# Kernel tuning notes

Hardware: AMD Instinct MI355X
Metric: run time of the kernel (lower is better)

## Reference

```python
import jax, jax.numpy as jnp
import numpy as np

P = 16; D = 1024; NH = 16; MAG = 4
B = 2; V = 4; H = 256; W = 512
DEPTH = 6; NE = 2; NM = 3   # dense-early, sparse-middle, rest dense-late
L = (H // P) * (W // P)    # 512 tokens
KEEP = L // 4              # keep_ratio = 0.25 -> 128 hard tokens
HD = D // NH
SCALE = HD ** -0.5


def setup_inputs() -> dict:
    key = jax.random.key(0)
    ks = iter(jax.random.split(key, 64))
    def rn(shape, s=0.02):
        return jax.random.normal(next(ks), shape, jnp.float32) * s
    inp = {}
    inp['x'] = jax.random.normal(next(ks), (B, V, H, W), jnp.float32)
    # select_hard_tokens: per-row randperm(L)[:K], sorted -> deterministic input
    rng = np.random.default_rng(0)
    hi = np.stack([np.sort(rng.permutation(L)[:KEEP]) for _ in range(B)]).astype(np.int32)
    inp['hard_idx'] = jnp.asarray(hi)
    inp['patch_w'] = rn((V, P * P, D)); inp['patch_b'] = jnp.zeros((V, D), jnp.float32)
    inp['var_embed'] = rn((V, D)); inp['var_query'] = rn((D,))
    inp['agg_wq'] = rn((D, D)); inp['agg_wk'] = rn((D, D))
    inp['agg_wv'] = rn((D, D)); inp['agg_wo'] = rn((D, D))
    inp['agg_bo'] = jnp.zeros((D,), jnp.float32)
    inp['pos_embed'] = rn((L, D), 1.0)
    inp['ln1_w'] = jnp.ones((DEPTH, D), jnp.float32); inp['ln1_b'] = jnp.zeros((DEPTH, D), jnp.float32)
    inp['qkv_w'] = rn((DEPTH, D, 3 * D)); inp['qkv_b'] = jnp.zeros((DEPTH, 3 * D), jnp.float32)
    inp['aproj_w'] = rn((DEPTH, D, D)); inp['aproj_b'] = jnp.zeros((DEPTH, D), jnp.float32)
    inp['ln2_w'] = jnp.ones((DEPTH, D), jnp.float32); inp['ln2_b'] = jnp.zeros((DEPTH, D), jnp.float32)
    inp['fc1_w'] = rn((DEPTH, D, 4 * D)); inp['fc1_b'] = jnp.zeros((DEPTH, 4 * D), jnp.float32)
    inp['fc2_w'] = rn((DEPTH, 4 * D, D)); inp['fc2_b'] = jnp.zeros((DEPTH, D), jnp.float32)
    inp['norm_w'] = jnp.ones((D,), jnp.float32); inp['norm_b'] = jnp.zeros((D,), jnp.float32)
    inp['head_w'] = rn((2, D, D)); inp['head_b'] = jnp.zeros((2, D), jnp.float32)
    inp['head_out_w'] = rn((D, (MAG * P) ** 2)); inp['head_out_b'] = jnp.zeros(((MAG * P) ** 2,), jnp.float32)
    inp['p2c1_w'] = rn((4 * MAG * MAG, V, 3, 3)); inp['p2c1_b'] = jnp.zeros((4 * MAG * MAG,), jnp.float32)
    inp['p2c2_w'] = rn((1, 4, 3, 3)); inp['p2c2_b'] = jnp.zeros((1,), jnp.float32)
    inp['cout_w'] = rn((1, 1, 3, 3)); inp['cout_b'] = jnp.zeros((1,), jnp.float32)
    return inp


def _ln(x, g, b):
    m = jnp.mean(x, -1, keepdims=True)
    v = jnp.mean((x - m) ** 2, -1, keepdims=True)
    return (x - m) * jax.lax.rsqrt(v + 1e-5) * g + b


def _conv3x3(x, w, b):
    y = jax.lax.conv_general_dilated(x, w, (1, 1), 'SAME',
                                     dimension_numbers=('NCHW', 'OIHW', 'NCHW'))
    return y + b[None, :, None, None]


def _pixel_shuffle(x, r):
    b, c, h, w = x.shape
    c2 = c // (r * r)
    return x.reshape(b, c2, r, r, h, w).transpose(0, 1, 4, 2, 5, 3).reshape(b, c2, h * r, w * r)


def _block_step(c, p):
    l1w, l1b, qw, qb, pw, pb, l2w, l2b, f1w, f1b, f2w, f2b = p
    bsz, n, _ = c.shape
    hn = _ln(c, l1w, l1b)
    qkv = (hn @ qw + qb).reshape(bsz, n, 3, NH, HD).transpose(2, 0, 3, 1, 4)  # 3,b,h,n,d
    qh, kh, vh = qkv[0], qkv[1], qkv[2]
    att = jax.nn.softmax(jnp.einsum('bhqd,bhkd->bhqk', qh, kh) * SCALE, axis=-1)
    o = jnp.einsum('bhqk,bhkd->bhqd', att, vh).transpose(0, 2, 1, 3).reshape(bsz, n, D)
    c = c + o @ pw + pb
    hn2 = _ln(c, l2w, l2b)
    c = c + jax.nn.gelu(hn2 @ f1w + f1b, approximate=False) @ f2w + f2b
    return c, None


def reference(x, hard_idx, patch_w, patch_b, var_embed, var_query,
              agg_wq, agg_wk, agg_wv, agg_wo, agg_bo, pos_embed,
              ln1_w, ln1_b, qkv_w, qkv_b, aproj_w, aproj_b,
              ln2_w, ln2_b, fc1_w, fc1_b, fc2_w, fc2_b,
              norm_w, norm_b, head_w, head_b, head_out_w, head_out_b,
              p2c1_w, p2c1_b, p2c2_w, p2c2_b, cout_w, cout_b):
    b_, v_, h_img, w_img = x.shape
    hh, ww = h_img // P, w_img // P
    ltok = hh * ww
    # per-variable patch embedding (PatchEmbed with in_chans=1)
    xp = x.reshape(b_, v_, hh, P, ww, P).transpose(0, 1, 2, 4, 3, 5).reshape(b_, v_, ltok, P * P)
    tok = jnp.einsum('bvle,ved->bvld', xp, patch_w) + patch_b[None, :, None, :]
    tok = tok + var_embed[None, :, None, :]
    # aggregate_variables: cross-attention query over V per token
    xf = tok.transpose(0, 2, 1, 3).reshape(b_ * ltok, v_, D)
    q = (var_query @ agg_wq).reshape(NH, HD)
    k = (xf @ agg_wk).reshape(-1, v_, NH, HD)
    vv = (xf @ agg_wv).reshape(-1, v_, NH, HD)
    a = jax.nn.softmax(jnp.einsum('hd,nvhd->nhv', q, k) * SCALE, axis=-1)
    agg = jnp.einsum('nhv,nvhd->nhd', a, vv).reshape(-1, D) @ agg_wo + agg_bo
    xt = agg.reshape(b_, ltok, D) + pos_embed[None]
    stacked = (ln1_w, ln1_b, qkv_w, qkv_b, aproj_w, aproj_b,
               ln2_w, ln2_b, fc1_w, fc1_b, fc2_w, fc2_b)
    def run(c, s, e):
        c, _ = jax.lax.scan(_block_step, c, tuple(ar[s:e] for ar in stacked))
        return c
    # dense early blocks (all tokens)
    xt = run(xt, 0, NE)
    # gather hard tokens -> sparse middle blocks; easy tokens skip via identity
    hard = jnp.take_along_axis(xt, hard_idx[:, :, None].astype(jnp.int32), axis=1)
    hard = run(hard, NE, NE + NM)
    brow = jnp.arange(b_)[:, None]
    xt = xt.at[brow, hard_idx].set(hard)  # merge_tokens (easy = identity)
    # dense late blocks
    xt = run(xt, NE + NM, DEPTH)
    xt = _ln(xt, norm_w, norm_b)
    # decoder head
    for i in range(head_w.shape[0]):
        xt = jax.nn.gelu(xt @ head_w[i] + head_b[i], approximate=False)
    pred = xt @ head_out_w + head_out_b  # (B, L, (MAG*P)^2)
    # unpatchify with scaling=MAG
    h2, w2 = h_img * MAG // P, w_img * MAG // P
    y = pred.reshape(b_, h2, w2, P, P, 1)
    y = jnp.einsum('nhwpqc->nchpwq', y).reshape(b_, 1, h2 * P, w2 * P)
    # residual path2 on raw input channels (out_var_index = all 4 channels here)
    r = jax.nn.gelu(_conv3x3(x, p2c1_w, p2c1_b), approximate=False)
    r = _pixel_shuffle(r, MAG)
    r = _conv3x3(r, p2c2_w, p2c2_b)
    return _conv3x3(y + r, cout_w, cout_b)
```

## Files before the change

### kernel.cpp

```cpp
#include <hip/hip_runtime.h>
#include <math.h>


#define UNIT 1048576L

typedef __attribute__((ext_vector_type(8))) short short8;
typedef __attribute__((ext_vector_type(4))) float f32x4;

#define GLDS(gp, lp) __builtin_amdgcn_global_load_lds( \
    (const __attribute__((address_space(1))) void*)(gp), \
    (__attribute__((address_space(3))) void*)(lp), 16, 0, 0)

__device__ __forceinline__ float gelu_f(float v){
  return 0.5f*v*(1.0f + erff(v*0.70710678118654752440f));
}

__device__ __forceinline__ unsigned short f2bf(float f){
  union { float f; unsigned u; } a; a.f = f;
  unsigned r = a.u + 0x7fffu + ((a.u >> 16) & 1u);
  return (unsigned short)(r >> 16);
}
__device__ __forceinline__ float bf2f(unsigned short u){
  union { unsigned u; float f; } a; a.u = (unsigned)u << 16;
  return a.f;
}

struct WJobs {
  const float* W[4];
  unsigned short* T[4];
  int K[4], N[4];
  int start[4];
};

__global__ __launch_bounds__(256)
void wtrans_multi(WJobs J)
{
  __shared__ float tile[32][33];
  int bx = blockIdx.x;
  int j = 0;
  #pragma unroll
  for (int i = 1; i < 4; ++i) if (bx >= J.start[i]) j = i;
  int local = bx - J.start[j];
  int K = J.K[j], N = J.N[j];
  int nx = N >> 5, tpb = (K >> 5) * nx;
  int bz = local / tpb, rem = local % tpb;
  int k0 = (rem / nx) * 32, n0 = (rem % nx) * 32;
  const float* Wp = J.W[j] + (long)bz * K * N;
  unsigned short* Wo = J.T[j] + (long)bz * K * N;
  int tx = threadIdx.x & 31, ty = threadIdx.x >> 5;
  #pragma unroll
  for (int i = 0; i < 4; ++i)
    tile[ty*4+i][tx] = Wp[(long)(k0 + ty*4 + i)*N + n0 + tx];
  __syncthreads();
  #pragma unroll
  for (int i = 0; i < 4; ++i){
    int n = ty*4 + i;
    Wo[(long)(n0 + n)*K + k0 + tx] = f2bf(tile[tx][n]);
  }
}

template<int TM>
__global__ __launch_bounds__(256)
void gemm_bt(const unsigned short* __restrict__ A, const unsigned short* __restrict__ Wt,
             const float* __restrict__ bias, const float* __restrict__ res,
             float* __restrict__ Cf, unsigned short* __restrict__ Cb,
             float* __restrict__ Cp, long MN, int splits,
             int M, int N, int K, int ldc,
             long sA, long sW, long sBias, long sRes, long sC,
             int wmod, int act)
{
  constexpr int NJ = (TM == 128) ? 4 : 2;
  int bz0 = blockIdx.z;
  int sp = bz0 % splits, bz = bz0 / splits;
  A += (long)bz * sA;
  int wb = bz % wmod;
  Wt += (long)wb * sW;
  const float* bptr = bias ? bias + (long)wb * sBias : nullptr;
  const float* rptr = res  ? res  + (long)bz * sRes : nullptr;
  if (Cf) Cf += (long)bz * sC;
  if (Cb) Cb += (long)bz * sC;

  __shared__ __align__(16) unsigned short As[TM*32];
  __shared__ __align__(16) unsigned short Bs[128*32];

  int t = threadIdx.x;
  int wave = t >> 6, lane = t & 63;
  int ln = lane & 15, kg = lane >> 4;
  int wm, wn;
  if (TM == 128){ wm = (wave & 1) * 64; wn = (wave >> 1) * 64; }
  else          { wm = 0;               wn = wave * 32; }
  int row0 = blockIdx.y * TM, col0 = blockIdx.x * 128;

  f32x4 acc[4][NJ];
  f32x4 z = {0.f, 0.f, 0.f, 0.f};
  #pragma unroll
  for (int i = 0; i < 4; ++i)
    #pragma unroll
    for (int j = 0; j < NJ; ++j) acc[i][j] = z;

  int sm = t >> 2;
  int sk = (t & 3) * 8;
  unsigned short* AsB = As + wave*512;
  unsigned short* BsB = Bs + wave*512;

  int kpb = K / splits;
  int kbeg = sp * kpb, kend = kbeg + kpb;
  for (int k0 = kbeg; k0 < kend; k0 += 32){
    if (TM == 128){
      GLDS(&A[(long)(row0 + sm)*K + k0 + sk],      AsB);
      GLDS(&A[(long)(row0 + 64 + sm)*K + k0 + sk], AsB + 2048);
    } else {
      GLDS(&A[(long)(row0 + sm)*K + k0 + sk],      AsB);
    }
    GLDS(&Wt[(long)(col0 + sm)*K + k0 + sk],      BsB);
    GLDS(&Wt[(long)(col0 + 64 + sm)*K + k0 + sk], BsB + 2048);
    __syncthreads();
    short8 af[4], bfg[NJ];
    #pragma unroll
    for (int i = 0; i < 4; ++i)  af[i]  = *(const short8*)&As[(wm + i*16 + ln)*32 + kg*8];
    #pragma unroll
    for (int j = 0; j < NJ; ++j) bfg[j] = *(const short8*)&Bs[(wn + j*16 + ln)*32 + kg*8];
    #pragma unroll
    for (int i = 0; i < 4; ++i)
      #pragma unroll
      for (int j = 0; j < NJ; ++j)
        acc[i][j] = __builtin_amdgcn_mfma_f32_16x16x32_bf16(af[i], bfg[j], acc[i][j], 0, 0, 0);
    __syncthreads();
  }

  if (Cp){
    long nbat = gridDim.z / splits;
    float* P = Cp + ((long)sp*nbat + bz)*MN;
    #pragma unroll
    for (int i = 0; i < 4; ++i){
      int rbase = row0 + wm + i*16 + kg*4;
      #pragma unroll
      for (int j = 0; j < NJ; ++j){
        int c = col0 + wn + j*16 + ln;
        #pragma unroll
        for (int rr2 = 0; rr2 < 4; ++rr2)
          P[(long)(rbase + rr2)*ldc + c] = acc[i][j][rr2];
      }
    }
    return;
  }
  #pragma unroll
  for (int i = 0; i < 4; ++i){
    int rbase = row0 + wm + i*16 + kg*4;
    #pragma unroll
    for (int j = 0; j < NJ; ++j){
      int c = col0 + wn + j*16 + ln;
      float bv = bptr ? bptr[c] : 0.f;
      #pragma unroll
      for (int rr2 = 0; rr2 < 4; ++rr2){
        int rrow = rbase + rr2;
        float v = acc[i][j][rr2] + bv;
        if (rptr) v += rptr[(long)rrow*ldc + c];
        if (act == 1) v = gelu_f(v);
        if (Cf) Cf[(long)rrow*ldc + c] = v;
        if (Cb) Cb[(long)rrow*ldc + c] = f2bf(v);
      }
    }
  }
}

__global__ __launch_bounds__(256)
void reduce_ep(const float* __restrict__ Cp, int splits, int nbat, long MN, int N,
               const float* __restrict__ bias, const float* __restrict__ res, long sRes,
               float* __restrict__ Cf, unsigned short* __restrict__ Cb, long sC, int act)
{
  long e4 = (long)blockIdx.x*256 + threadIdx.x;
  if (e4 >= (long)nbat*MN/4) return;
  long e = e4 * 4;
  int b = (int)(e / MN); long r = e % MN; int col = (int)(r % N);
  float4 s = *(const float4*)&Cp[(long)b*MN + r];
  for (int sp = 1; sp < splits; ++sp){
    float4 p = *(const float4*)&Cp[((long)sp*nbat + b)*MN + r];
    s.x += p.x; s.y += p.y; s.z += p.z; s.w += p.w;
  }
  if (bias){
    float4 bv = *(const float4*)&bias[col];
    s.x += bv.x; s.y += bv.y; s.z += bv.z; s.w += bv.w;
  }
  if (res){
    float4 rv = *(const float4*)&res[(long)b*sRes + r];
    s.x += rv.x; s.y += rv.y; s.z += rv.z; s.w += rv.w;
  }
  if (act == 1){
    s.x = gelu_f(s.x); s.y = gelu_f(s.y); s.z = gelu_f(s.z); s.w = gelu_f(s.w);
  }
  if (Cf) *(float4*)&Cf[(long)b*sC + r] = s;
  if (Cb){
    unsigned q0 = (unsigned)f2bf(s.x) | ((unsigned)f2bf(s.y) << 16);
    unsigned q1 = (unsigned)f2bf(s.z) | ((unsigned)f2bf(s.w) << 16);
    uint2 pk = {q0, q1};
    *(uint2*)&Cb[(long)b*sC + r] = pk;
  }
}

__global__ __launch_bounds__(256)
void ln_bf(const float* __restrict__ x, const float* __restrict__ g,
           const float* __restrict__ b, unsigned short* __restrict__ y)
{
  long r = blockIdx.x;
  int t = threadIdx.x;
  float4 v = ((const float4*)(x + r*1024))[t];
  float s  = v.x + v.y + v.z + v.w;
  float ss = v.x*v.x + v.y*v.y + v.z*v.z + v.w*v.w;
  #pragma unroll
  for (int o = 32; o; o >>= 1){ s += __shfl_xor(s, o); ss += __shfl_xor(ss, o); }
  __shared__ float sa[4], sb[4];
  int w = t >> 6, lane = t & 63;
  if (!lane){ sa[w] = s; sb[w] = ss; }
  __syncthreads();
  s  = sa[0] + sa[1] + sa[2] + sa[3];
  ss = sb[0] + sb[1] + sb[2] + sb[3];
  float mean = s * (1.0f/1024.0f);
  float var  = ss * (1.0f/1024.0f) - mean*mean;
  float rstd = rsqrtf(var + 1e-5f);
  float4 gv = ((const float4*)g)[t];
  float4 bv = ((const float4*)b)[t];
  float ox = (v.x-mean)*rstd*gv.x + bv.x;
  float oy = (v.y-mean)*rstd*gv.y + bv.y;
  float oz = (v.z-mean)*rstd*gv.z + bv.z;
  float ow = (v.w-mean)*rstd*gv.w + bv.w;
  unsigned q0 = (unsigned)f2bf(ox) | ((unsigned)f2bf(oy) << 16);
  unsigned q1 = (unsigned)f2bf(oz) | ((unsigned)f2bf(ow) << 16);
  uint2 pk = {q0, q1};
  *(uint2*)&y[r*1024 + t*4] = pk;
}

__global__ void xp_extract(const float* __restrict__ x, unsigned short* __restrict__ xp)
{
  int idx = blockIdx.x * 256 + threadIdx.x;
  int e4 = idx & 63;
  int lt = (idx >> 6) & 511;
  int zz = idx >> 15;
  int e  = e4 << 2;
  int py = e >> 4, px0 = e & 15;
  int hy = lt >> 5, wx = lt & 31;
  float4 v = *(const float4*)&x[((long)zz*256 + hy*16 + py)*512 + wx*16 + px0];
  unsigned q0 = (unsigned)f2bf(v.x) | ((unsigned)f2bf(v.y) << 16);
  unsigned q1 = (unsigned)f2bf(v.z) | ((unsigned)f2bf(v.w) << 16);
  uint2 pk = {q0, q1};
  ((uint2*)xp)[idx] = pk;
}

__global__ void pb2_combine(const float* __restrict__ pb, const float* __restrict__ ve,
                            float* __restrict__ out)
{
  int i = blockIdx.x * 256 + threadIdx.x;
  out[i] = pb[i] + ve[i];
}

__global__ void qproj(const float* __restrict__ vq, const float* __restrict__ wq,
                      float* __restrict__ q)
{
  int n = blockIdx.x * 64 + threadIdx.x;
  float s = 0.f;
  for (int k = 0; k < 1024; ++k) s += vq[k] * wq[(long)k*1024 + n];
  q[n] = s;
}

__global__ void wk_fold(const float* __restrict__ wk, const float* __restrict__ qv,
                        float* __restrict__ wt)
{
  int i = blockIdx.x * 256 + threadIdx.x;
  int h = i & 15, D = i >> 4;
  const float* wr = wk + (long)D*1024 + h*64;
  const float* qr = qv + h*64;
  float s = 0.f;
  #pragma unroll
  for (int d = 0; d < 64; ++d) s += wr[d]*qr[d];
  wt[h*1024 + D] = s;
}

__global__ __launch_bounds__(64)
void agg_attn2(const unsigned short* __restrict__ tok, const float* __restrict__ vb,
               const float* __restrict__ wt, unsigned short* __restrict__ out)
{
  int l = blockIdx.x, h = blockIdx.y, b = blockIdx.z, t = threadIdx.x;
  const float* wh = wt + h*1024;
  float sc[4];
  #pragma unroll
  for (int v = 0; v < 4; ++v){
    const unsigned short* tr = tok + ((((long)b*4 + v)*512 + l) << 10);
    float s = 0.f;
    #pragma unroll
    for (int j = 0; j < 16; ++j){
      int D = t + j*64;
      s += bf2f(tr[D]) * wh[D];
    }
    #pragma unroll
    for (int o = 32; o; o >>= 1) s += __shfl_xor(s, o);
    sc[v] = s * 0.125f;
  }
  float m = fmaxf(fmaxf(sc[0], sc[1]), fmaxf(sc[2], sc[3]));
  float e0 = __expf(sc[0]-m), e1 = __expf(sc[1]-m), e2 = __expf(sc[2]-m), e3 = __expf(sc[3]-m);
  float inv = 1.0f / (e0 + e1 + e2 + e3);
  long base = (((long)b*4)*512 + l)*1024 + h*64 + t;
  float o = e0*vb[base] + e1*vb[base + 512*1024] + e2*vb[base + 2*512*1024] + e3*vb[base + 3*512*1024];
  out[(((long)b*512 + l) << 10) + h*64 + t] = f2bf(o * inv);
}

__global__ __launch_bounds__(256)
void attn_v2(const float* __restrict__ qkv, unsigned short* __restrict__ out, int N)
{
  int h = blockIdx.y, b = blockIdx.z;
  int row0 = blockIdx.x * 32;
  int t = threadIdx.x;
  int r = t & 31, g = t >> 5;
  int c0 = g * 8;
  const float* base = qkv + (long)b * N * 3072;

  __shared__ float QsT[64][33];
  __shared__ float KV[64][68];
  __shared__ float Ps[32][65];
  __shared__ float red[32][9], red2[32][9];

  {
    const float* qp = base + (long)(row0 + r)*3072 + h*64 + c0;
    float4 a  = *(const float4*)qp;
    float4 bq = *(const float4*)(qp + 4);
    QsT[c0+0][r]=a.x;  QsT[c0+1][r]=a.y;  QsT[c0+2][r]=a.z;  QsT[c0+3][r]=a.w;
    QsT[c0+4][r]=bq.x; QsT[c0+5][r]=bq.y; QsT[c0+6][r]=bq.z; QsT[c0+7][r]=bq.w;
  }
  float m_r = -1e30f, l_r = 0.f;
  float O[8] = {0,0,0,0,0,0,0,0};
  int vc = t & 63, vd = (t >> 6) * 16;

  for (int j0 = 0; j0 < N; j0 += 64){
    __syncthreads();
    {
      const float* kp = base + (long)(j0 + vc)*3072 + 1024 + h*64 + vd;
      float4 k1 = *(const float4*)kp,     k2 = *(const float4*)(kp+4);
      float4 k3 = *(const float4*)(kp+8), k4 = *(const float4*)(kp+12);
      KV[vd+ 0][vc]=k1.x; KV[vd+ 1][vc]=k1.y; KV[vd+ 2][vc]=k1.z; KV[vd+ 3][vc]=k1.w;
      KV[vd+ 4][vc]=k2.x; KV[vd+ 5][vc]=k2.y; KV[vd+ 6][vc]=k2.z; KV[vd+ 7][vc]=k2.w;
      KV[vd+ 8][vc]=k3.x; KV[vd+ 9][vc]=k3.y; KV[vd+10][vc]=k3.z; KV[vd+11][vc]=k3.w;
      KV[vd+12][vc]=k4.x; KV[vd+13][vc]=k4.y; KV[vd+14][vc]=k4.z; KV[vd+15][vc]=k4.w;
    }
    __syncthreads();
    float s[8] = {0,0,0,0,0,0,0,0};
    #pragma unroll 16
    for (int d = 0; d < 64; ++d){
      float q = QsT[d][r];
      float4 k1 = *(const float4*)&KV[d][c0];
      float4 k2 = *(const float4*)&KV[d][c0+4];
      s[0] += q*k1.x; s[1] += q*k1.y; s[2] += q*k1.z; s[3] += q*k1.w;
      s[4] += q*k2.x; s[5] += q*k2.y; s[6] += q*k2.z; s[7] += q*k2.w;
    }
    float lm = -1e30f;
    #pragma unroll
    for (int i = 0; i < 8; ++i){ s[i] *= 0.125f; lm = fmaxf(lm, s[i]); }
    red[r][g] = lm;
    __syncthreads();
    float mc = red[r][0];
    #pragma unroll
    for (int gg = 1; gg < 8; ++gg) mc = fmaxf(mc, red[r][gg]);
    float m_new = fmaxf(m_r, mc);
    float alpha = __expf(m_r - m_new);
    float ls = 0.f;
    #pragma unroll
    for (int i = 0; i < 8; ++i){ float p = __expf(s[i]-m_new); Ps[r][c0+i] = p; ls += p; }
    red2[r][g] = ls;
    __syncthreads();
    float cs = 0.f;
    #pragma unroll
    for (int gg = 0; gg < 8; ++gg) cs += red2[r][gg];
    l_r = alpha*l_r + cs;
    m_r = m_new;
    #pragma unroll
    for (int i = 0; i < 8; ++i) O[i] *= alpha;
    {
      const float* vp = base + (long)(j0 + vc)*3072 + 2048 + h*64 + vd;
      float4 v1 = *(const float4*)vp,     v2 = *(const float4*)(vp+4);
      float4 v3 = *(const float4*)(vp+8), v4 = *(const float4*)(vp+12);
      *(float4*)&KV[vc][vd]    = v1;
      *(float4*)&KV[vc][vd+4]  = v2;
      *(float4*)&KV[vc][vd+8]  = v3;
      *(float4*)&KV[vc][vd+12] = v4;
    }
    __syncthreads();
    #pragma unroll 16
    for (int j = 0; j < 64; ++j){
      float p = Ps[r][j];
      float4 v1 = *(const float4*)&KV[j][c0];
      float4 v2 = *(const float4*)&KV[j][c0+4];
      O[0] += p*v1.x; O[1] += p*v1.y; O[2] += p*v1.z; O[3] += p*v1.w;
      O[4] += p*v2.x; O[5] += p*v2.y; O[6] += p*v2.z; O[7] += p*v2.w;
    }
  }
  float inv = 1.0f / l_r;
  unsigned q0 = (unsigned)f2bf(O[0]*inv) | ((unsigned)f2bf(O[1]*inv) << 16);
  unsigned q1 = (unsigned)f2bf(O[2]*inv) | ((unsigned)f2bf(O[3]*inv) << 16);
  unsigned q2 = (unsigned)f2bf(O[4]*inv) | ((unsigned)f2bf(O[5]*inv) << 16);
  unsigned q3 = (unsigned)f2bf(O[6]*inv) | ((unsigned)f2bf(O[7]*inv) << 16);
  uint4 pk = {q0, q1, q2, q3};
  *(uint4*)&out[((long)(b*N + row0 + r))*1024 + h*64 + c0] = pk;
}

__global__ __launch_bounds__(256)
void gather_rows(const float* __restrict__ src, const int* __restrict__ idx,
                 float* __restrict__ dst)
{
  int r = blockIdx.x;
  int b = r >> 7, i = r & 127;
  int s = idx[b*128 + i];
  ((float4*)(dst + (long)r*1024))[threadIdx.x] =
      ((const float4*)(src + ((long)b*512 + s)*1024))[threadIdx.x];
}
__global__ __launch_bounds__(256)
void scatter_rows(const float* __restrict__ src, const int* __restrict__ idx,
                  float* __restrict__ dst)
{
  int r = blockIdx.x;
  int b = r >> 7, i = r & 127;
  int s = idx[b*128 + i];
  ((float4*)(dst + ((long)b*512 + s)*1024))[threadIdx.x] =
      ((const float4*)(src + (long)r*1024))[threadIdx.x];
}

__global__ __launch_bounds__(256)
void conv1_v4(const float* __restrict__ x, const float* __restrict__ w,
              const float* __restrict__ bi, unsigned short* __restrict__ out)
{
  __shared__ unsigned short obuf[256*68];
  int t = threadIdx.x;
  int id = blockIdx.x*256 + t;
  int px = id & 511, py = (id >> 9) & 255, bb = id >> 17;
  float in[4][9];
  #pragma unroll
  for (int ci = 0; ci < 4; ++ci){
    const float* xc = x + ((long)(bb*4 + ci)*256)*512;
    #pragma unroll
    for (int ky = 0; ky < 3; ++ky){
      int yy = py + ky - 1;
      #pragma unroll
      for (int kx = 0; kx < 3; ++kx){
        int xx = px + kx - 1;
        bool ok = ((unsigned)yy < 256u) && ((unsigned)xx < 512u);
        in[ci][ky*3+kx] = ok ? xc[yy*512 + xx] : 0.f;
      }
    }
  }
  unsigned short* orow = &obuf[t*68];
  #pragma unroll 2
  for (int g = 0; g < 8; ++g){
    unsigned pk[4];
    #pragma unroll
    for (int u = 0; u < 8; ++u){
      int co = g*8 + u;
      float s = bi[co];
      #pragma unroll
      for (int ci = 0; ci < 4; ++ci){
        const float* wc = w + (co*4 + ci)*9;
        #pragma unroll
        for (int k = 0; k < 9; ++k) s += in[ci][k]*wc[k];
      }
      s = gelu_f(s);
      unsigned short h = f2bf(s);
      if (u & 1) pk[u>>1] |= ((unsigned)h << 16);
      else       pk[u>>1]  = (unsigned)h;
    }
    uint2 v0 = {pk[0], pk[1]};
    uint2 v1 = {pk[2], pk[3]};
    *(uint2*)&orow[g*8]     = v0;
    *(uint2*)&orow[g*8 + 4] = v1;
  }
  __syncthreads();
  unsigned short* ob = out + (long)blockIdx.x * (256*64);
  #pragma unroll
  for (int j = 0; j < 8; ++j){
    int u = j*256 + t;
    int p = u >> 3, s4 = u & 7;
    uint2 a  = *(const uint2*)&obuf[p*68 + s4*8];
    uint2 b2 = *(const uint2*)&obuf[p*68 + s4*8 + 4];
    uint4 v = {a.x, a.y, b2.x, b2.y};
    *(uint4*)&ob[(long)u*8] = v;
  }
}

__global__ __launch_bounds__(256)
void conv2_v3(const unsigned short* __restrict__ r1, const float* __restrict__ w,
              const float* __restrict__ bi, float* __restrict__ out)
{
  __shared__ float cbuf[108*68];
  int X0 = blockIdx.x*64, Y0 = blockIdx.y*16, bb = blockIdx.z;
  int cx0 = (X0 >> 2) - 1, cy0 = (Y0 >> 2) - 1;
  int t = threadIdx.x;
  const unsigned short* rb = r1 + (long)bb*256*512*64;
  for (int i4 = t; i4 < 1728; i4 += 256){
    int cell = i4 >> 4, ch4 = (i4 & 15) << 2;
    int cy = cy0 + cell/18, cx = cx0 + cell%18;
    float4 v = {0.f, 0.f, 0.f, 0.f};
    if ((unsigned)cy < 256u && (unsigned)cx < 512u){
      uint2 u = *(const uint2*)&rb[(((long)cy*512 + cx) << 6) + ch4];
      v.x = bf2f((unsigned short)(u.x & 0xffff));
      v.y = bf2f((unsigned short)(u.x >> 16));
      v.z = bf2f((unsigned short)(u.y & 0xffff));
      v.w = bf2f((unsigned short)(u.y >> 16));
    }
    *(float4*)&cbuf[cell*68 + ch4] = v;
  }
  float wv[36];
  #pragma unroll
  for (int k = 0; k < 36; ++k) wv[k] = w[k];
  float bias = bi[0];
  __syncthreads();
  int lx = t & 63, tq = t >> 6;
  int X = X0 + lx;
  #pragma unroll
  for (int j = 0; j < 4; ++j){
    int Y = Y0 + tq*4 + j;
    float s = bias;
    #pragma unroll
    for (int ky = 0; ky < 3; ++ky){
      int yy = Y + ky - 1;
      if ((unsigned)yy >= 1024u) continue;
      int ly = (yy >> 2) - cy0, phy = (yy & 3) << 2;
      #pragma unroll
      for (int kx = 0; kx < 3; ++kx){
        int xx = X + kx - 1;
        if ((unsigned)xx >= 2048u) continue;
        int lxc = (xx >> 2) - cx0;
        const float* cp = &cbuf[(ly*18 + lxc)*68 + phy + (xx & 3)];
        s += cp[0]*wv[ky*3+kx] + cp[16]*wv[9+ky*3+kx]
           + cp[32]*wv[18+ky*3+kx] + cp[48]*wv[27+ky*3+kx];
      }
    }
    out[(((long)bb*1024 + Y) << 11) + X] = s;
  }
}

__global__ __launch_bounds__(256)
void cout_fused(const float* __restrict__ pred, const float* __restrict__ r2,
                const float* __restrict__ w, const float* __restrict__ bi,
                float* __restrict__ out)
{
  __shared__ float tb[18*66];
  int X0 = blockIdx.x*64, Y0 = blockIdx.y*16, bb = blockIdx.z;
  int t = threadIdx.x;
  for (int i = t; i < 1188; i += 256){
    int ly = i/66, lx = i%66;
    int Y = Y0 + ly - 1, X = X0 + lx - 1;
    float v = 0.f;
    if ((unsigned)Y < 1024u && (unsigned)X < 2048u){
      int i2 = Y >> 4, p = Y & 15, j2 = X >> 4, q = X & 15;
      int l = i2*8 + (j2 >> 4);
      int e = ((j2 & 15) << 8) + (p << 4) + q;
      v = pred[(((long)bb*512 + l) << 12) + e] + r2[(((long)bb*1024 + Y) << 11) + X];
    }
    tb[i] = v;
  }
  float w0=w[0], w1=w[1], w2=w[2], w3=w[3], w4=w[4], w5=w[5], w6=w[6], w7=w[7], w8=w[8];
  float bias = bi[0];
  __syncthreads();
  int lx = t & 63, tq = t >> 6;
  #pragma unroll
  for (int j = 0; j < 4; ++j){
    int ry = tq*4 + j;
    const float* c = &tb[ry*66 + lx];
    float s = bias + c[0]*w0 + c[1]*w1 + c[2]*w2
            + c[66]*w3 + c[67]*w4 + c[68]*w5
            + c[132]*w6 + c[133]*w7 + c[134]*w8;
    out[(((long)bb*1024 + Y0 + ry) << 11) + X0 + lx] = s;
  }
}

static inline void gemm_go(hipStream_t st, int TM, const unsigned short* A,
                           const unsigned short* Wt,
                           const float* bias, const float* res, float* Cf, unsigned short* Cb,
                           float* Cp, int splits,
                           int M, int N, int K, int batches,
                           long sA, long sW, long sBias, long sRes, long sC,
                           int wmod, int act)
{
  dim3 g(N/128, M/TM, batches*splits);
  long MN = (long)M*N;
  if (TM == 128)
    gemm_bt<128><<<g, 256, 0, st>>>(A, Wt, bias, res, Cf, Cb, Cp, MN, splits,
                                    M, N, K, N, sA, sW, sBias, sRes, sC, wmod, act);
  else
    gemm_bt<64><<<g, 256, 0, st>>>(A, Wt, bias, res, Cf, Cb, Cp, MN, splits,
                                   M, N, K, N, sA, sW, sBias, sRes, sC, wmod, act);
}

static inline void reduce_go(hipStream_t st, const float* Cp, int splits, int nbat,
                             long MN, int N, const float* bias, const float* res, long sRes,
                             float* Cf, unsigned short* Cb, long sC, int act)
{
  long total4 = (long)nbat*MN/4;
  reduce_ep<<<(int)((total4 + 255)/256), 256, 0, st>>>(Cp, splits, nbat, MN, N,
                                                       bias, res, sRes, Cf, Cb, sC, act);
}

static inline void wmulti_go(hipStream_t st, int njobs,
                             const float* W0, unsigned short* T0, int K0, int N0, int nb0,
                             const float* W1, unsigned short* T1, int K1, int N1, int nb1,
                             const float* W2, unsigned short* T2, int K2, int N2, int nb2,
                             const float* W3, unsigned short* T3, int K3, int N3, int nb3)
{
  WJobs J;
  const float* Ws[4] = {W0, W1, W2, W3};
  unsigned short* Ts[4] = {T0, T1, T2, T3};
  int Ks[4] = {K0, K1, K2, K3}, Ns[4] = {N0, N1, N2, N3}, nbs[4] = {nb0, nb1, nb2, nb3};
  int acc = 0;
  for (int i = 0; i < 4; ++i){
    if (i < njobs){
      J.W[i] = Ws[i]; J.T[i] = Ts[i]; J.K[i] = Ks[i]; J.N[i] = Ns[i];
      J.start[i] = acc;
      acc += nbs[i] * (Ks[i] >> 5) * (Ns[i] >> 5);
    } else {
      J.W[i] = Ws[0]; J.T[i] = Ts[0]; J.K[i] = 32; J.N[i] = 32;
      J.start[i] = 0x7fffffff;
    }
  }
  wtrans_multi<<<acc, 256, 0, st>>>(J);
}

extern "C" void kernel_launch(void* const* d_in, const int* in_sizes, int n_in,
                              void* d_out, int out_size, void* d_ws, size_t ws_size,
                              hipStream_t stream)
{
  const float* x         = (const float*)d_in[0];
  const int*   hard_idx  = (const int*)  d_in[1];
  const float* patch_w   = (const float*)d_in[2];
  const float* patch_b   = (const float*)d_in[3];
  const float* var_embed = (const float*)d_in[4];
  const float* var_query = (const float*)d_in[5];
  const float* agg_wq    = (const float*)d_in[6];
  const float* agg_wk    = (const float*)d_in[7];
  const float* agg_wv    = (const float*)d_in[8];
  const float* agg_wo    = (const float*)d_in[9];
  const float* agg_bo    = (const float*)d_in[10];
  const float* pos_embed = (const float*)d_in[11];
  const float* ln1_w     = (const float*)d_in[12];
  const float* ln1_b     = (const float*)d_in[13];
  const float* qkv_w     = (const float*)d_in[14];
  const float* qkv_b     = (const float*)d_in[15];
  const float* aproj_w   = (const float*)d_in[16];
  const float* aproj_b   = (const float*)d_in[17];
  const float* ln2_w     = (const float*)d_in[18];
  const float* ln2_b     = (const float*)d_in[19];
  const float* fc1_w     = (const float*)d_in[20];
  const float* fc1_b     = (const float*)d_in[21];
  const float* fc2_w     = (const float*)d_in[22];
  const float* fc2_b     = (const float*)d_in[23];
  const float* norm_w    = (const float*)d_in[24];
  const float* norm_b    = (const float*)d_in[25];
  const float* head_w    = (const float*)d_in[26];
  const float* head_b    = (const float*)d_in[27];
  const float* head_out_w= (const float*)d_in[28];
  const float* head_out_b= (const float*)d_in[29];
  const float* p2c1_w    = (const float*)d_in[30];
  const float* p2c1_b    = (const float*)d_in[31];
  const float* p2c2_w    = (const float*)d_in[32];
  const float* p2c2_b    = (const float*)d_in[33];
  const float* cout_w    = (const float*)d_in[34];
  const float* cout_b    = (const float*)d_in[35];

  float* ws = (float*)d_ws;
  float* xt   = ws;
  float* r2   = ws + 1*UNIT;
  float* qkvb = ws + 5*UNIT;
  float* pred = ws + 8*UNIT;
  unsigned short* rbig = (unsigned short*)(ws + 8*UNIT);
  float* vb   = ws + 12*UNIT;
  float* Cp   = ws + 12*UNIT;
  unsigned short* b16 = (unsigned short*)(ws + 16*UNIT);
  unsigned short* hn_bf    = b16;
  unsigned short* ao_bf    = b16 + 1*UNIT;
  unsigned short* ff_bf    = b16 + 2*UNIT;
  unsigned short* xp_bf    = b16 + 6*UNIT;
  unsigned short* tok_bf   = b16 + 7*UNIT;
  unsigned short* aggin_bf = b16 + 11*UNIT;
  unsigned short* wt_a     = b16 + 12*UNIT;
  float* tail = ws + 28*UNIT;
  float* pb2  = tail;
  float* qv   = tail + 4096;
  float* wtl  = tail + 5120;
  float* hbuf = tail + 21504;

  conv1_v4<<<1024, 256, 0, stream>>>(x, p2c1_w, p2c1_b, rbig);
  conv2_v3<<<dim3(32, 64, 2), 256, 0, stream>>>(rbig, p2c2_w, p2c2_b, r2);

  unsigned short* wt_patch = wt_a;
  unsigned short* wt_wv    = wt_a + 1*UNIT;
  unsigned short* wt_wo    = wt_a + 2*UNIT;
  pb2_combine<<<16, 256, 0, stream>>>(patch_b, var_embed, pb2);
  xp_extract<<<1024, 256, 0, stream>>>(x, xp_bf);
  qproj<<<16, 64, 0, stream>>>(var_query, agg_wq, qv);
  wk_fold<<<64, 256, 0, stream>>>(agg_wk, qv, wtl);
  wmulti_go(stream, 3,
            patch_w, wt_patch, 256, 1024, 4,
            agg_wv,  wt_wv,   1024, 1024, 1,
            agg_wo,  wt_wo,   1024, 1024, 1,
            nullptr, nullptr, 0, 0, 0);
  gemm_go(stream, 128, xp_bf, wt_patch, pb2, nullptr, nullptr, tok_bf, nullptr, 1,
          512, 1024, 256, 8, 512L*256, 256L*1024, 1024, 0, 512L*1024, 4, 0);
  gemm_go(stream, 128, tok_bf, wt_wv, nullptr, nullptr, vb, nullptr, nullptr, 1,
          512, 1024, 1024, 8, 512L*1024, 0, 0, 0, 512L*1024, 1, 0);
  agg_attn2<<<dim3(512, 16, 2), 64, 0, stream>>>(tok_bf, vb, wtl, aggin_bf);
  gemm_go(stream, 64, aggin_bf, wt_wo, nullptr, nullptr, nullptr, nullptr, Cp, 2,
          512, 1024, 1024, 2, 512L*1024, 0, 0, 0, 512L*1024, 1, 0);
  reduce_go(stream, Cp, 2, 2, 512L*1024, 1024, agg_bo, pos_embed, 0, xt, nullptr,
            512L*1024, 0);

  unsigned short* wt_qkv   = wt_a;
  unsigned short* wt_aproj = wt_a + 3*UNIT;
  unsigned short* wt_fc1   = wt_a + 4*UNIT;
  unsigned short* wt_fc2   = wt_a + 8*UNIT;

  auto run_block = [&](float* cur, int Nt, int d){
    int rows = 2 * Nt;
    bool dense = (rows >= 1024);
    int TMbig = dense ? 128 : 64;
    long MNq = (long)rows*3072, MNa = (long)rows*1024, MNf = (long)rows*4096;
    wmulti_go(stream, 4,
              qkv_w   + (long)d*1024*3072, wt_qkv,   1024, 3072, 1,
              aproj_w + (long)d*1024*1024, wt_aproj, 1024, 1024, 1,
              fc1_w   + (long)d*1024*4096, wt_fc1,   1024, 4096, 1,
              fc2_w   + (long)d*4096*1024, wt_fc2,   4096, 1024, 1);
    ln_bf<<<rows, 256, 0, stream>>>(cur, ln1_w + d*1024, ln1_b + d*1024, hn_bf);
    gemm_go(stream, TMbig, hn_bf, wt_qkv, qkv_b + d*3072, nullptr, qkvb, nullptr, nullptr, 1,
            rows, 3072, 1024, 1, 0, 0, 0, 0, 0, 1, 0);
    attn_v2<<<dim3(Nt/32, 16, 2), 256, 0, stream>>>(qkvb, ao_bf, Nt);
    {
      int sk = dense ? 4 : 8;
      gemm_go(stream, TMbig, ao_bf, wt_aproj, nullptr, nullptr, nullptr, nullptr, Cp, sk,
              rows, 1024, 1024, 1, 0, 0, 0, 0, 0, 1, 0);
      reduce_go(stream, Cp, sk, 1, MNa, 1024, aproj_b + d*1024, cur, MNa, cur, nullptr, MNa, 0);
    }
    ln_bf<<<rows, 256, 0, stream>>>(cur, ln2_w + d*1024, ln2_b + d*1024, hn_bf);
    if (dense){
      gemm_go(stream, 128, hn_bf, wt_fc1, fc1_b + d*4096, nullptr, nullptr, ff_bf, nullptr, 1,
              rows, 4096, 1024, 1, 0, 0, 0, 0, 0, 1, 1);
    } else {
      gemm_go(stream, 64, hn_bf, wt_fc1, nullptr, nullptr, nullptr, nullptr, Cp, 2,
              rows, 4096, 1024, 1, 0, 0, 0, 0, 0, 1, 1);
      reduce_go(stream, Cp, 2, 1, MNf, 4096, fc1_b + d*4096, nullptr, 0, nullptr, ff_bf, MNf, 1);
    }
    {
      int sk = dense ? 4 : 8;
      gemm_go(stream, TMbig, ff_bf, wt_fc2, nullptr, nullptr, nullptr, nullptr, Cp, sk,
              rows, 1024, 4096, 1, 0, 0, 0, 0, 0, 1, 0);
      reduce_go(stream, Cp, sk, 1, MNa, 1024, fc2_b + d*1024, cur, MNa, cur, nullptr, MNa, 0);
    }
  };

  run_block(xt, 512, 0);
  run_block(xt, 512, 1);
  gather_rows<<<256, 256, 0, stream>>>(xt, hard_idx, hbuf);
  run_block(hbuf, 128, 2);
  run_block(hbuf, 128, 3);
  run_block(hbuf, 128, 4);
  scatter_rows<<<256, 256, 0, stream>>>(hbuf, hard_idx, xt);
  run_block(xt, 512, 5);

  unsigned short* wt_h1 = wt_a;
  unsigned short* wt_h2 = wt_a + 1*UNIT;
  unsigned short* wt_ho = wt_a + 2*UNIT;
  wmulti_go(stream, 3,
            head_w,              wt_h1, 1024, 1024, 1,
            head_w + 1024L*1024, wt_h2, 1024, 1024, 1,
            head_out_w,          wt_ho, 1024, 4096, 1,
            nullptr, nullptr, 0, 0, 0);
  ln_bf<<<1024, 256, 0, stream>>>(xt, norm_w, norm_b, hn_bf);
  gemm_go(stream, 64, hn_bf, wt_h1, nullptr, nullptr, nullptr, nullptr, Cp, 2,
          1024, 1024, 1024, 1, 0, 0, 0, 0, 0, 1, 1);
  reduce_go(stream, Cp, 2, 1, 1024L*1024, 1024, head_b, nullptr, 0, nullptr, ao_bf,
            1024L*1024, 1);
  gemm_go(stream, 64, ao_bf, wt_h2, nullptr, nullptr, nullptr, nullptr, Cp, 2,
          1024, 1024, 1024, 1, 0, 0, 0, 0, 0, 1, 1);
  reduce_go(stream, Cp, 2, 1, 1024L*1024, 1024, head_b + 1024, nullptr, 0, nullptr, hn_bf,
            1024L*1024, 1);
  gemm_go(stream, 128, hn_bf, wt_ho, head_out_b, nullptr, pred, nullptr, nullptr, 1,
          1024, 4096, 1024, 1, 0, 0, 0, 0, 0, 1, 0);

  cout_fused<<<dim3(32, 64, 2), 256, 0, stream>>>(pred, r2, cout_w, cout_b, (float*)d_out);
}
```

Baseline: 1.574 ms.

## Rewrite attention with bf16 MFMA and split-KV across waves

Replaces the scalar fp32 flash-attention kernel with one that converts Q, K and V to bf16 and computes QK^T and PV with 16x16x32 MFMA instructions. Each block processes 128-key tiles, and pairs of waves split the key range; their partial softmax states are merged through shared memory at the end. This removes the fp32 FMA inner loops and several block-wide reductions per tile. In exchange it adds bf16 rounding of the attention inputs and probabilities, plus a strided transpose store of V into LDS that may cause bank conflicts.

```diff
diff --git a/kernel.cpp b/kernel.cpp
--- a/kernel.cpp
+++ b/kernel.cpp
@@ -304,100 +304,155 @@
 }
 
 __global__ __launch_bounds__(256)
-void attn_v2(const float* __restrict__ qkv, unsigned short* __restrict__ out, int N)
+void attn_mfma(const float* __restrict__ qkv, unsigned short* __restrict__ out, int N)
 {
   int h = blockIdx.y, b = blockIdx.z;
   int row0 = blockIdx.x * 32;
   int t = threadIdx.x;
-  int r = t & 31, g = t >> 5;
-  int c0 = g * 8;
+  int wave = t >> 6, lane = t & 63;
+  int ln = lane & 15, kg = lane >> 4;
+  int mtile = wave & 1, khalf = wave >> 1;
   const float* base = qkv + (long)b * N * 3072;
 
-  __shared__ float QsT[64][33];
-  __shared__ float KV[64][68];
-  __shared__ float Ps[32][65];
-  __shared__ float red[32][9], red2[32][9];
-
+  __shared__ __align__(16) unsigned short Ks[128*72];
+  __shared__ __align__(16) unsigned short Vt[64*136];
+  __shared__ __align__(16) unsigned short Pw[4][16*72];
+  __shared__ float Obuf[4][16][68];
+  __shared__ float Mbuf[4][16], Lbuf[4][16];
+
+  short8 qf[2];
   {
-    const float* qp = base + (long)(row0 + r)*3072 + h*64 + c0;
-    float4 a  = *(const float4*)qp;
-    float4 bq = *(const float4*)(qp + 4);
-    QsT[c0+0][r]=a.x;  QsT[c0+1][r]=a.y;  QsT[c0+2][r]=a.z;  QsT[c0+3][r]=a.w;
-    QsT[c0+4][r]=bq.x; QsT[c0+5][r]=bq.y; QsT[c0+6][r]=bq.z; QsT[c0+7][r]=bq.w;
-  }
-  float m_r = -1e30f, l_r = 0.f;
-  float O[8] = {0,0,0,0,0,0,0,0};
-  int vc = t & 63, vd = (t >> 6) * 16;
-
-  for (int j0 = 0; j0 < N; j0 += 64){
+    const float* qp = base + (long)(row0 + mtile*16 + ln)*3072 + h*64;
+    #pragma unroll
+    for (int s = 0; s < 2; ++s){
+      float4 a = *(const float4*)(qp + s*32 + kg*8);
+      float4 c = *(const float4*)(qp + s*32 + kg*8 + 4);
+      short8 q;
+      q[0] = (short)f2bf(a.x*0.125f); q[1] = (short)f2bf(a.y*0.125f);
+      q[2] = (short)f2bf(a.z*0.125f); q[3] = (short)f2bf(a.w*0.125f);
+      q[4] = (short)f2bf(c.x*0.125f); q[5] = (short)f2bf(c.y*0.125f);
+      q[6] = (short)f2bf(c.z*0.125f); q[7] = (short)f2bf(c.w*0.125f);
+      qf[s] = q;
+    }
+  }
+
+  f32x4 z = {0.f, 0.f, 0.f, 0.f};
+  f32x4 O[4] = {z, z, z, z};
+  float mrow[4] = {-1e30f, -1e30f, -1e30f, -1e30f};
+  float lrow[4] = {0.f, 0.f, 0.f, 0.f};
+  unsigned short* pw = &Pw[wave][0];
+
+  for (int j0 = 0; j0 < N; j0 += 128){
+    #pragma unroll
+    for (int it = 0; it < 2; ++it){
+      int key = (t >> 2) + it*64;
+      int dg = (t & 3) * 16;
+      const float* kp = base + (long)(j0 + key)*3072 + 1024 + h*64 + dg;
+      float4 k0 = *(const float4*)kp,     k1 = *(const float4*)(kp+4);
+      float4 k2 = *(const float4*)(kp+8), k3 = *(const float4*)(kp+12);
+      unsigned short* kd = &Ks[key*72 + dg];
+      uint2 p0 = { (unsigned)f2bf(k0.x) | ((unsigned)f2bf(k0.y)<<16),
+                   (unsigned)f2bf(k0.z) | ((unsigned)f2bf(k0.w)<<16) };
+      uint2 p1 = { (unsigned)f2bf(k1.x) | ((unsigned)f2bf(k1.y)<<16),
+                   (unsigned)f2bf(k1.z) | ((unsigned)f2bf(k1.w)<<16) };
+      uint2 p2 = { (unsigned)f2bf(k2.x) | ((unsigned)f2bf(k2.y)<<16),
+                   (unsigned)f2bf(k2.z) | ((unsigned)f2bf(k2.w)<<16) };
+      uint2 p3 = { (unsigned)f2bf(k3.x) | ((unsigned)f2bf(k3.y)<<16),
+                   (unsigned)f2bf(k3.z) | ((unsigned)f2bf(k3.w)<<16) };
+      *(uint2*)&kd[0]  = p0; *(uint2*)&kd[4]  = p1;
+      *(uint2*)&kd[8]  = p2; *(uint2*)&kd[12] = p3;
+      const float* vp = base + (long)(j0 + key)*3072 + 2048 + h*64 + dg;
+      float4 v0 = *(const float4*)vp,     v1 = *(const float4*)(vp+4);
+      float4 v2 = *(const float4*)(vp+8), v3 = *(const float4*)(vp+12);
+      float vv[16];
+      vv[0]=v0.x; vv[1]=v0.y; vv[2]=v0.z; vv[3]=v0.w;
+      vv[4]=v1.x; vv[5]=v1.y; vv[6]=v1.z; vv[7]=v1.w;
+      vv[8]=v2.x; vv[9]=v2.y; vv[10]=v2.z; vv[11]=v2.w;
+      vv[12]=v3.x; vv[13]=v3.y; vv[14]=v3.z; vv[15]=v3.w;
+      #pragma unroll
+      for (int i = 0; i < 16; ++i) Vt[(dg+i)*136 + key] = f2bf(vv[i]);
+    }
     __syncthreads();
-    {
-      const float* kp = base + (long)(j0 + vc)*3072 + 1024 + h*64 + vd;
-      float4 k1 = *(const float4*)kp,     k2 = *(const float4*)(kp+4);
-      float4 k3 = *(const float4*)(kp+8), k4 = *(const float4*)(kp+12);
-      KV[vd+ 0][vc]=k1.x; KV[vd+ 1][vc]=k1.y; KV[vd+ 2][vc]=k1.z; KV[vd+ 3][vc]=k1.w;
-      KV[vd+ 4][vc]=k2.x; KV[vd+ 5][vc]=k2.y; KV[vd+ 6][vc]=k2.z; KV[vd+ 7][vc]=k2.w;
-      KV[vd+ 8][vc]=k3.x; KV[vd+ 9][vc]=k3.y; KV[vd+10][vc]=k3.z; KV[vd+11][vc]=k3.w;
-      KV[vd+12][vc]=k4.x; KV[vd+13][vc]=k4.y; KV[vd+14][vc]=k4.z; KV[vd+15][vc]=k4.w;
+
+    f32x4 acc[4] = {z, z, z, z};
+    const unsigned short* kbase = &Ks[(khalf*64)*72];
+    #pragma unroll
+    for (int s = 0; s < 2; ++s){
+      #pragma unroll
+      for (int nt = 0; nt < 4; ++nt){
+        short8 bf = *(const short8*)&kbase[(nt*16 + ln)*72 + s*32 + kg*8];
+        acc[nt] = __builtin_amdgcn_mfma_f32_16x16x32_bf16(qf[s], bf, acc[nt], 0, 0, 0);
+      }
+    }
+
+    #pragma unroll
+    for (int r = 0; r < 4; ++r){
+      float mt = fmaxf(fmaxf(acc[0][r], acc[1][r]), fmaxf(acc[2][r], acc[3][r]));
+      #pragma unroll
+      for (int o = 1; o < 16; o <<= 1) mt = fmaxf(mt, __shfl_xor(mt, o));
+      float m_new = fmaxf(mrow[r], mt);
+      float alpha = __expf(mrow[r] - m_new);
+      float ps = 0.f;
+      #pragma unroll
+      for (int nt = 0; nt < 4; ++nt){
+        float p = __expf(acc[nt][r] - m_new);
+        ps += p;
+        pw[(kg*4 + r)*72 + nt*16 + ln] = f2bf(p);
+      }
+      #pragma unroll
+      for (int o = 1; o < 16; o <<= 1) ps += __shfl_xor(ps, o);
+      lrow[r] = alpha*lrow[r] + ps;
+      mrow[r] = m_new;
+      O[0][r] *= alpha; O[1][r] *= alpha; O[2][r] *= alpha; O[3][r] *= alpha;
+    }
+
+    #pragma unroll
+    for (int s = 0; s < 2; ++s){
+      short8 pa = *(const short8*)&pw[ln*72 + s*32 + kg*8];
+      #pragma unroll
+      for (int dt = 0; dt < 4; ++dt){
+        short8 bv = *(const short8*)&Vt[(dt*16 + ln)*136 + khalf*64 + s*32 + kg*8];
+        O[dt] = __builtin_amdgcn_mfma_f32_16x16x32_bf16(pa, bv, O[dt], 0, 0, 0);
+      }
     }
     __syncthreads();
-    float s[8] = {0,0,0,0,0,0,0,0};
-    #pragma unroll 16
-    for (int d = 0; d < 64; ++d){
-      float q = QsT[d][r];
-      float4 k1 = *(const float4*)&KV[d][c0];
-      float4 k2 = *(const float4*)&KV[d][c0+4];
-      s[0] += q*k1.x; s[1] += q*k1.y; s[2] += q*k1.z; s[3] += q*k1.w;
-      s[4] += q*k2.x; s[5] += q*k2.y; s[6] += q*k2.z; s[7] += q*k2.w;
-    }
-    float lm = -1e30f;
-    #pragma unroll
-    for (int i = 0; i < 8; ++i){ s[i] *= 0.125f; lm = fmaxf(lm, s[i]); }
-    red[r][g] = lm;
-    __syncthreads();
-    float mc = red[r][0];
-    #pragma unroll
-    for (int gg = 1; gg < 8; ++gg) mc = fmaxf(mc, red[r][gg]);
-    float m_new = fmaxf(m_r, mc);
-    float alpha = __expf(m_r - m_new);
-    float ls = 0.f;
-    #pragma unroll
-    for (int i = 0; i < 8; ++i){ float p = __expf(s[i]-m_new); Ps[r][c0+i] = p; ls += p; }
-    red2[r][g] = ls;
-    __syncthreads();
-    float cs = 0.f;
-    #pragma unroll
-    for (int gg = 0; gg < 8; ++gg) cs += red2[r][gg];
-    l_r = alpha*l_r + cs;
-    m_r = m_new;
-    #pragma unroll
-    for (int i = 0; i < 8; ++i) O[i] *= alpha;
-    {
-      const float* vp = base + (long)(j0 + vc)*3072 + 2048 + h*64 + vd;
-      float4 v1 = *(const float4*)vp,     v2 = *(const float4*)(vp+4);
-      float4 v3 = *(const float4*)(vp+8), v4 = *(const float4*)(vp+12);
-      *(float4*)&KV[vc][vd]    = v1;
-      *(float4*)&KV[vc][vd+4]  = v2;
-      *(float4*)&KV[vc][vd+8]  = v3;
-      *(float4*)&KV[vc][vd+12] = v4;
-    }
-    __syncthreads();
-    #pragma unroll 16
-    for (int j = 0; j < 64; ++j){
-      float p = Ps[r][j];
-      float4 v1 = *(const float4*)&KV[j][c0];
-      float4 v2 = *(const float4*)&KV[j][c0+4];
-      O[0] += p*v1.x; O[1] += p*v1.y; O[2] += p*v1.z; O[3] += p*v1.w;
-      O[4] += p*v2.x; O[5] += p*v2.y; O[6] += p*v2.z; O[7] += p*v2.w;
-    }
-  }
-  float inv = 1.0f / l_r;
-  unsigned q0 = (unsigned)f2bf(O[0]*inv) | ((unsigned)f2bf(O[1]*inv) << 16);
-  unsigned q1 = (unsigned)f2bf(O[2]*inv) | ((unsigned)f2bf(O[3]*inv) << 16);
-  unsigned q2 = (unsigned)f2bf(O[4]*inv) | ((unsigned)f2bf(O[5]*inv) << 16);
-  unsigned q3 = (unsigned)f2bf(O[6]*inv) | ((unsigned)f2bf(O[7]*inv) << 16);
+  }
+
+  #pragma unroll
+  for (int dt = 0; dt < 4; ++dt)
+    #pragma unroll
+    for (int r = 0; r < 4; ++r)
+      Obuf[wave][kg*4 + r][dt*16 + ln] = O[dt][r];
+  if (ln == 0){
+    #pragma unroll
+    for (int r = 0; r < 4; ++r){
+      Mbuf[wave][kg*4 + r] = mrow[r];
+      Lbuf[wave][kg*4 + r] = lrow[r];
+    }
+  }
+  __syncthreads();
+  int row = t >> 3, d0 = (t & 7) * 8;
+  int wa = row >> 4, lr = row & 15;
+  float ma = Mbuf[wa][lr],  mb2 = Mbuf[wa+2][lr];
+  float la = Lbuf[wa][lr],  lb  = Lbuf[wa+2][lr];
+  float mm = fmaxf(ma, mb2);
+  float ea = __expf(ma - mm), eb = __expf(mb2 - mm);
+  float linv = 1.0f / (la*ea + lb*eb);
+  ea *= linv; eb *= linv;
+  float4 a0 = *(const float4*)&Obuf[wa][lr][d0];
+  float4 a1 = *(const float4*)&Obuf[wa][lr][d0+4];
+  float4 b0 = *(const float4*)&Obuf[wa+2][lr][d0];
+  float4 b1 = *(const float4*)&Obuf[wa+2][lr][d0+4];
+  float o0 = a0.x*ea + b0.x*eb, o1 = a0.y*ea + b0.y*eb;
+  float o2 = a0.z*ea + b0.z*eb, o3 = a0.w*ea + b0.w*eb;
+  float o4 = a1.x*ea + b1.x*eb, o5 = a1.y*ea + b1.y*eb;
+  float o6 = a1.z*ea + b1.z*eb, o7 = a1.w*ea + b1.w*eb;
+  unsigned q0 = (unsigned)f2bf(o0) | ((unsigned)f2bf(o1) << 16);
+  unsigned q1 = (unsigned)f2bf(o2) | ((unsigned)f2bf(o3) << 16);
+  unsigned q2 = (unsigned)f2bf(o4) | ((unsigned)f2bf(o5) << 16);
+  unsigned q3 = (unsigned)f2bf(o6) | ((unsigned)f2bf(o7) << 16);
   uint4 pk = {q0, q1, q2, q3};
-  *(uint4*)&out[((long)(b*N + row0 + r))*1024 + h*64 + c0] = pk;
+  *(uint4*)&out[((long)(b*N + row0 + row))*1024 + h*64 + d0] = pk;
 }
 
 __global__ __launch_bounds__(256)
@@ -725,7 +780,7 @@
     ln_bf<<<rows, 256, 0, stream>>>(cur, ln1_w + d*1024, ln1_b + d*1024, hn_bf);
     gemm_go(stream, TMbig, hn_bf, wt_qkv, qkv_b + d*3072, nullptr, qkvb, nullptr, nullptr, 1,
             rows, 3072, 1024, 1, 0, 0, 0, 0, 0, 1, 0);
-    attn_v2<<<dim3(Nt/32, 16, 2), 256, 0, stream>>>(qkvb, ao_bf, Nt);
+    attn_mfma<<<dim3(Nt/32, 16, 2), 256, 0, stream>>>(qkvb, ao_bf, Nt);
     {
       int sk = dense ? 4 : 8;
       gemm_go(stream, TMbig, ao_bf, wt_aproj, nullptr, nullptr, nullptr, nullptr, Cp, sk,
```

Measured after the change: 1.373 ms. -12.8%, faster.
